# Performance work log

Measured on AMD Instinct MI355X. Metric: run time of the kernel, lower is better.

## Reference

```python
import jax, jax.numpy as jnp
import numpy as np

SCORE_THRESH = 0.05
NMS_THRESH = 0.5
MAX_DET = 100
N_BOXES = 8192


def setup_inputs() -> dict:
    key = jax.random.key(0)
    k1, k2, k3, k4, k5 = jax.random.split(key, 5)
    N = N_BOXES
    # well-formed axis-aligned boxes (x1,y1,x2,y2) plus 8 keypoint coords
    xy = jax.random.uniform(k1, (N, 2)) * 1000.0
    wh = jax.random.uniform(k2, (N, 2)) * 120.0 + 4.0
    kp = jax.random.uniform(k3, (N, 8)) * 1000.0
    boxes = jnp.concatenate([xy, xy + wh, kp], axis=1)            # (N, 12)
    classification = jax.random.uniform(k4, (N, 8))               # two heads x 4 orientations
    dimensions = jax.random.uniform(k5, (N, 3)) * 4.0             # (h, w, l) for the single class
    return {"boxes": boxes, "dimensions": dimensions, "classification": classification}


def _nms_keep(b4, scores, valid):
    """Greedy NMS. Returns (order, keep) where order sorts by score desc and
    keep[i] says whether the i-th sorted box survives."""
    N = b4.shape[0]
    order = jnp.argsort(-jnp.where(valid, scores, -jnp.inf))
    bs = b4[order]                                                 # (N, 4) sorted boxes
    vs = valid[order]
    x1, y1, x2, y2 = bs[:, 0], bs[:, 1], bs[:, 2], bs[:, 3]
    area = (x2 - x1) * (y2 - y1)
    iw = jnp.clip(jnp.minimum(x2[:, None], x2[None, :]) - jnp.maximum(x1[:, None], x1[None, :]), 0.0)
    ih = jnp.clip(jnp.minimum(y2[:, None], y2[None, :]) - jnp.maximum(y1[:, None], y1[None, :]), 0.0)
    inter = iw * ih                                                # (N, N)
    iou = inter / jnp.maximum(area[:, None] + area[None, :] - inter, 1e-8)
    idx = jnp.arange(N)

    def body(keep, xs):
        row, v, i = xs
        suppressed = jnp.any(keep & (row > NMS_THRESH) & (idx < i))
        keep = keep.at[i].set(v & jnp.logical_not(suppressed))
        return keep, None

    keep, _ = jax.lax.scan(body, jnp.zeros((N,), dtype=bool), (iou, vs, idx))
    return order, keep


def reference(boxes, dimensions, classification):
    # max over the two classification heads -> per-orientation score (N, 4)
    cls2 = jnp.maximum(classification[:, :4], classification[:, 4:])
    orient = jnp.argmax(cls2, axis=1)                              # best orientation per box
    score = jnp.max(cls2, axis=1)                                  # best-orientation score
    valid = score > SCORE_THRESH

    order, keep = _nms_keep(boxes[:, :4], score, valid)
    sorted_score = jnp.where(keep, score[order], -jnp.inf)
    top_scores, top_pos = jax.lax.top_k(sorted_score, MAX_DET)     # top-k among kept
    sel = order[top_pos]                                           # original box indices
    ok = jnp.isfinite(top_scores)                                  # real detections vs -1 padding

    out_boxes = jnp.where(ok[:, None], boxes[sel], -1.0)           # (MAX_DET, 12)
    out_dims = jnp.where(ok[:, None], dimensions[sel, :3], -1.0)   # (MAX_DET, 3)
    out_scores = jnp.where(ok, score[sel], -1.0)                   # (MAX_DET,)
    out_labels = jnp.where(ok, 0, -1).astype(jnp.int32)            # single class -> label 0
    out_orient = jnp.where(ok, orient[sel], -1).astype(jnp.int32)
    return out_boxes, out_dims, out_scores, out_labels, out_orient
```

## Files before the change

### kernel.cpp

```cpp
#include <hip/hip_runtime.h>

#define NBOX 8192
#define BT 1024
#define MAXDET 100
#define SCORE_T 0.05f
#define NMS_T 0.5f
#define CAP 1024
#define KTGT 128
#define TOPBIN_T 0.99609375f

typedef unsigned long long u64;

__device__ __forceinline__ float rl_f(float v, int j) {
    return __int_as_float(__builtin_amdgcn_readlane(__float_as_int(v), j));
}

__device__ __forceinline__ float iou_fn(float x1, float y1, float x2, float y2, float area,
                                        float bx1, float by1, float bx2, float by2, float barea) {
    float iw = fminf(x2, bx2) - fmaxf(x1, bx1);
    float ih = fminf(y2, by2) - fmaxf(y1, by1);
    iw = fmaxf(iw, 0.0f);
    ih = fmaxf(ih, 0.0f);
    float inter = iw * ih;
    return inter / fmaxf(area + barea - inter, 1e-8f);
}

__device__ __forceinline__ void bins_of(unsigned k, int& b1, int& b2) {
    float s = __uint_as_float(k & 0x7FFFFFFFu);
    b1 = (int)(s * 256.0f); if (b1 > 255) b1 = 255;
    b2 = (int)(s * 65536.0f) & 255;
}

__global__ __launch_bounds__(BT) void filterdet_kernel(
    const float* __restrict__ boxes, const float* __restrict__ dims,
    const float* __restrict__ cls, float* __restrict__ out) {
    __shared__ unsigned s_key[NBOX];
    __shared__ unsigned s_hist[256];
    __shared__ u64 s_sel[CAP];
    __shared__ u64 s_srt[CAP];
    __shared__ unsigned short s_srtpos[CAP];
    __shared__ float4 s_cb[CAP];
    __shared__ float4 s_bb[128];
    __shared__ float s_bar[128];
    __shared__ float4 s_kb[MAXDET];
    __shared__ float s_karea[MAXDET], s_kscore[MAXDET];
    __shared__ int s_ksel[MAXDET];
    __shared__ int s_kc, s_cnt, s_B1, s_B2, s_state, s_refKrem;
    __shared__ u64 s_alive0;

    const int tid = threadIdx.x;
    const int lane = tid & 63;
    const int wid = tid >> 6;

    auto rank_scatter = [&](int sc, bool loadBox) {
        if (tid < sc) {
            u64 mine = s_sel[tid];
            float4 pb = make_float4(0.f, 0.f, 0.f, 0.f);
            if (loadBox) {
                int bidx = NBOX - 1 - (int)(mine & 8191ull);
                pb = *reinterpret_cast<const float4*>(boxes + bidx * 12);
            }
            int rank = 0;
            int j = 0;
            for (; j + 8 <= sc; j += 8) {
                u64 a0 = s_sel[j + 0], a1 = s_sel[j + 1], a2 = s_sel[j + 2], a3 = s_sel[j + 3];
                u64 a4 = s_sel[j + 4], a5 = s_sel[j + 5], a6 = s_sel[j + 6], a7 = s_sel[j + 7];
                rank += (int)(a0 > mine) + (int)(a1 > mine) + (int)(a2 > mine) + (int)(a3 > mine)
                      + (int)(a4 > mine) + (int)(a5 > mine) + (int)(a6 > mine) + (int)(a7 > mine);
            }
            for (; j < sc; ++j) rank += (s_sel[j] > mine) ? 1 : 0;
            s_srt[rank] = mine;
            s_srtpos[rank] = (unsigned short)tid;
            if (loadBox) s_cb[tid] = pb;
        }
    };

    auto nms_groups = [&](int scN) {
        for (int base = 0; base < scN && s_kc < MAXDET; base += 128) {
            const int kc0 = s_kc;
            float x1 = 0.f, y1 = 0.f, x2 = 0.f, y2 = 0.f, area = 0.f, sscore = 0.f;
            int sidx = 0; bool have = false;
            if (wid < 2) {
                int p = base + wid * 64 + lane;
                have = p < scN;
                u64 v = have ? s_srt[p] : 0ull;
                int cp = have ? (int)s_srtpos[p] : 0;
                sidx = NBOX - 1 - (int)(v & 8191ull);
                sscore = __uint_as_float(((unsigned)(v >> 13)) & 0x7FFFFFFFu);
                float4 b = s_cb[cp];
                if (have) { x1 = b.x; y1 = b.y; x2 = b.z; y2 = b.w; area = (x2 - x1) * (y2 - y1); }
                int sl = wid * 64 + lane;
                s_bb[sl] = make_float4(x1, y1, x2, y2); s_bar[sl] = area;
            }
            __syncthreads();
            if (wid == 0) {
                bool cand = have;
                for (int k = 0; k < kc0; ++k) {
                    float4 kb = s_kb[k];
                    float iou = iou_fn(x1, y1, x2, y2, area, kb.x, kb.y, kb.z, kb.w, s_karea[k]);
                    cand = cand && !(iou > NMS_T);
                }
                u64 m = 0ull;
#pragma unroll 8
                for (int j = 0; j < 64; ++j) {
                    float iou = iou_fn(x1, y1, x2, y2, area,
                                       rl_f(x1, j), rl_f(y1, j), rl_f(x2, j), rl_f(y2, j), rl_f(area, j));
                    if ((iou > NMS_T) && (j < lane)) m |= (1ull << j);
                }
                u64 alive = __ballot(cand);
                u64 conf = __ballot((m & alive) != 0ull) & alive;
                while (conf) {
                    int i = (int)__builtin_ctzll(conf);
                    bool deadI = (lane == i) && ((m & alive) != 0ull);
                    u64 d = __ballot(deadI);
                    alive &= ~d; conf &= ~(d | (1ull << i));
                }
                int rank = (int)__popcll(alive & ((1ull << lane) - 1ull));
                int slot = kc0 + rank;
                if (((alive >> lane) & 1ull) && slot < MAXDET) {
                    s_kb[slot] = make_float4(x1, y1, x2, y2);
                    s_karea[slot] = area; s_kscore[slot] = sscore; s_ksel[slot] = sidx;
                }
                if (lane == 0) s_alive0 = alive;
            }
            u64 m_low = 0ull, m_high = 0ull;
            bool cand1 = have;
            if (wid == 1) {
                for (int k = 0; k < kc0; ++k) {
                    float4 kb = s_kb[k];
                    float iou = iou_fn(x1, y1, x2, y2, area, kb.x, kb.y, kb.z, kb.w, s_karea[k]);
                    cand1 = cand1 && !(iou > NMS_T);
                }
#pragma unroll 8
                for (int j = 0; j < 64; ++j) {
                    float4 bb = s_bb[j];
                    float iou = iou_fn(x1, y1, x2, y2, area, bb.x, bb.y, bb.z, bb.w, s_bar[j]);
                    if (iou > NMS_T) m_low |= (1ull << j);
                }
#pragma unroll 8
                for (int j = 0; j < 64; ++j) {
                    float iou = iou_fn(x1, y1, x2, y2, area,
                                       rl_f(x1, j), rl_f(y1, j), rl_f(x2, j), rl_f(y2, j), rl_f(area, j));
                    if ((iou > NMS_T) && (j < lane)) m_high |= (1ull << j);
                }
            }
            __syncthreads();
            if (wid == 1) {
                u64 alive0 = s_alive0;
                int popc0 = (int)__popcll(alive0);
                bool cand = cand1 && ((m_low & alive0) == 0ull);
                u64 alive = __ballot(cand);
                u64 conf = __ballot((m_high & alive) != 0ull) & alive;
                while (conf) {
                    int i = (int)__builtin_ctzll(conf);
                    bool deadI = (lane == i) && ((m_high & alive) != 0ull);
                    u64 d = __ballot(deadI);
                    alive &= ~d; conf &= ~(d | (1ull << i));
                }
                int rank = (int)__popcll(alive & ((1ull << lane) - 1ull));
                int slot = kc0 + popc0 + rank;
                if (((alive >> lane) & 1ull) && slot < MAXDET) {
                    s_kb[slot] = make_float4(x1, y1, x2, y2);
                    s_karea[slot] = area; s_kscore[slot] = sscore; s_ksel[slot] = sidx;
                }
                if (lane == 0) {
                    int nk = kc0 + popc0 + (int)__popcll(alive);
                    s_kc = nk > MAXDET ? MAXDET : nk;
                }
            }
            __syncthreads();
        }
    };

    unsigned keyr[8];
#pragma unroll
    for (int j = 0; j < 8; ++j) {
        int i = tid + j * BT;
        const float4 c0 = *reinterpret_cast<const float4*>(cls + i * 8);
        const float4 c1 = *reinterpret_cast<const float4*>(cls + i * 8 + 4);
        float s = fmaxf(fmaxf(fmaxf(c0.x, c1.x), fmaxf(c0.y, c1.y)),
                        fmaxf(fmaxf(c0.z, c1.z), fmaxf(c0.w, c1.w)));
        unsigned u = __float_as_uint(s);
        unsigned key = (u >> 31) ? ~u : (u | 0x80000000u);
        key = (s > SCORE_T) ? key : 0u;
        keyr[j] = key;
        s_key[i] = key;
    }
    if (tid == 0) { s_kc = 0; s_cnt = 0; }
    __syncthreads();
#pragma unroll
    for (int j = 0; j < 8; ++j) {
        unsigned k = keyr[j];
        if (k) {
            float s = __uint_as_float(k & 0x7FFFFFFFu);
            if (s >= TOPBIN_T) {
                int pos = atomicAdd(&s_cnt, 1);
                if (pos < CAP) {
                    int i = tid + j * BT;
                    s_sel[pos] = (((u64)k) << 13) | (unsigned)(NBOX - 1 - i);
                    s_cb[pos] = *reinterpret_cast<const float4*>(boxes + i * 12);
                }
            }
        }
    }
    __syncthreads();
    const int cnt0 = s_cnt;
    const bool ovf = cnt0 > CAP;

    if (!ovf && cnt0 > 0) {
        rank_scatter(cnt0, false);
        __syncthreads();
        nms_groups(cnt0);
    }

    int U1 = ovf ? 256 : 255;
    int U2 = 0;

    if (s_kc < MAXDET) {
        if (tid < 256) s_hist[tid] = 0u;
        if (tid == 0) s_cnt = 0;
        __syncthreads();
        for (int j = 0; j < NBOX / BT; ++j) {
            unsigned k = s_key[tid + j * BT];
            if (k) {
                int b1, b2; bins_of(k, b1, b2);
                if (b1 < U1 || (b1 == U1 && b2 < U2)) atomicAdd(&s_hist[b1], 1u);
            }
        }
        while (true) {
            __syncthreads();
            if (wid == 0) {
                unsigned c0 = s_hist[lane * 4 + 0], c1s = s_hist[lane * 4 + 1];
                unsigned c2 = s_hist[lane * 4 + 2], c3 = s_hist[lane * 4 + 3];
                unsigned t3 = c3, t2 = c2 + t3, t1 = c1s + t2, t0 = c0 + t1;
                unsigned acc = t0;
#pragma unroll
                for (int d = 1; d < 64; d <<= 1) {
                    unsigned o = __shfl_down(acc, d);
                    if (lane + d < 64) acc += o;
                }
                unsigned excl = acc - t0;
                unsigned totalRem = __shfl(acc, 0);
                if (lane == 0) s_state = (totalRem == 0u) ? 2 : 0;
                if (totalRem != 0u) {
                    unsigned Kt = totalRem < (unsigned)KTGT ? totalRem : (unsigned)KTGT;
                    unsigned incq[4] = { excl + t0, excl + t1, excl + t2, excl + t3 };
                    unsigned abvq[4] = { excl + t1, excl + t2, excl + t3, excl };
#pragma unroll
                    for (int q = 0; q < 4; ++q) {
                        if (incq[q] >= Kt && abvq[q] < Kt) {
                            s_B1 = lane * 4 + q; s_B2 = 0;
                            if (incq[q] > CAP) { s_state = 1; s_refKrem = (int)(Kt - abvq[q]); }
                        }
                    }
                }
            }
            __syncthreads();
            const int st = s_state;
            if (st == 2) break;
            const int B1 = s_B1;
            if (st == 1) {
                if (tid < 256) s_hist[tid] = 0u;
                __syncthreads();
                for (int j = 0; j < NBOX / BT; ++j) {
                    unsigned k = s_key[tid + j * BT];
                    if (k) {
                        int b1, b2; bins_of(k, b1, b2);
                        if ((b1 < U1 || (b1 == U1 && b2 < U2)) && b1 == B1)
                            atomicAdd(&s_hist[b2], 1u);
                    }
                }
                __syncthreads();
                if (wid == 0) {
                    unsigned c0 = s_hist[lane * 4 + 0], c1s = s_hist[lane * 4 + 1];
                    unsigned c2 = s_hist[lane * 4 + 2], c3 = s_hist[lane * 4 + 3];
                    unsigned t3 = c3, t2 = c2 + t3, t1 = c1s + t2, t0 = c0 + t1;
                    unsigned acc = t0;
#pragma unroll
                    for (int d = 1; d < 64; d <<= 1) {
                        unsigned o = __shfl_down(acc, d);
                        if (lane + d < 64) acc += o;
                    }
                    unsigned excl = acc - t0;
                    unsigned Krem = (unsigned)s_refKrem;
                    unsigned incq[4] = { excl + t0, excl + t1, excl + t2, excl + t3 };
                    unsigned abvq[4] = { excl + t1, excl + t2, excl + t3, excl };
#pragma unroll
                    for (int q = 0; q < 4; ++q)
                        if (incq[q] >= Krem && abvq[q] < Krem) s_B2 = lane * 4 + q;
                }
                __syncthreads();
            }
            const int B2 = s_B2;
            for (int j = 0; j < NBOX / BT; ++j) {
                int i = tid + j * BT;
                unsigned k = s_key[i];
                if (k) {
                    int b1, b2; bins_of(k, b1, b2);
                    bool inr = (b1 < U1) || (b1 == U1 && b2 < U2);
                    bool sel = inr && ((b1 > B1) || (b1 == B1 && b2 >= B2));
                    if (sel) {
                        int pos = atomicAdd(&s_cnt, 1);
                        if (pos < CAP)
                            s_sel[pos] = (((u64)k) << 13) | (unsigned)(NBOX - 1 - i);
                    }
                }
            }
            __syncthreads();
            const int sc2 = s_cnt < CAP ? s_cnt : CAP;
            rank_scatter(sc2, true);
            __syncthreads();
            nms_groups(sc2);
            if (s_kc >= MAXDET) break;
            U1 = B1; U2 = B2;
            if (tid < 256) s_hist[tid] = 0u;
            if (tid == 0) s_cnt = 0;
            __syncthreads();
            for (int j = 0; j < NBOX / BT; ++j) {
                unsigned k = s_key[tid + j * BT];
                if (k) {
                    int b1, b2; bins_of(k, b1, b2);
                    if (b1 < U1 || (b1 == U1 && b2 < U2)) atomicAdd(&s_hist[b1], 1u);
                }
            }
        }
    }
    __syncthreads();

    if (tid < MAXDET) {
        const int kc = s_kc;
        float* ob = out;
        float* od = out + MAXDET * 12;
        float* os = out + MAXDET * 15;
        float* ol = out + MAXDET * 16;
        float* oo = out + MAXDET * 17;
        float4* obr = reinterpret_cast<float4*>(ob + tid * 12);
        if (tid < kc) {
            int sel = s_ksel[tid];
            const float4* br = reinterpret_cast<const float4*>(boxes + sel * 12);
            obr[0] = br[0]; obr[1] = br[1]; obr[2] = br[2];
            od[tid * 3 + 0] = dims[sel * 3 + 0];
            od[tid * 3 + 1] = dims[sel * 3 + 1];
            od[tid * 3 + 2] = dims[sel * 3 + 2];
            os[tid] = s_kscore[tid];
            ol[tid] = 0.0f;
            const float4 c0 = *reinterpret_cast<const float4*>(cls + sel * 8);
            const float4 c1 = *reinterpret_cast<const float4*>(cls + sel * 8 + 4);
            float m0 = fmaxf(c0.x, c1.x);
            float m1 = fmaxf(c0.y, c1.y);
            float m2 = fmaxf(c0.z, c1.z);
            float m3 = fmaxf(c0.w, c1.w);
            int o = 0; float best = m0;
            if (m1 > best) { best = m1; o = 1; }
            if (m2 > best) { best = m2; o = 2; }
            if (m3 > best) { best = m3; o = 3; }
            oo[tid] = (float)o;
        } else {
            const float4 neg1 = make_float4(-1.f, -1.f, -1.f, -1.f);
            obr[0] = neg1; obr[1] = neg1; obr[2] = neg1;
            od[tid * 3 + 0] = -1.0f; od[tid * 3 + 1] = -1.0f; od[tid * 3 + 2] = -1.0f;
            os[tid] = -1.0f; ol[tid] = -1.0f; oo[tid] = -1.0f;
        }
    }
}

extern "C" void kernel_launch(void* const* d_in, const int* in_sizes, int n_in,
                              void* d_out, int out_size, void* d_ws, size_t ws_size,
                              hipStream_t stream) {
    const float* boxes = (const float*)d_in[0];
    const float* dims  = (const float*)d_in[1];
    const float* cls   = (const float*)d_in[2];
    float* out = (float*)d_out;
    (void)in_sizes; (void)n_in; (void)out_size; (void)d_ws; (void)ws_size;
    filterdet_kernel<<<1, BT, 0, stream>>>(boxes, dims, cls, out);
}
```

Baseline: 27.01 us.

## Split scoring into a multi-block prepass kernel and shrink the NMS kernel

Moves the per-box score/key computation and top-bin candidate compaction into a 64-block prepass kernel that writes keys, per-block counts, packed candidate keys, boxes, keypoints and dims/orientation to workspace. The single-block NMS kernel drops to 256 threads, prefix-sums the block counts to gather candidates, and emits outputs from the staged workspace arrays. The aim is to spread the global-memory-bound scoring pass across many CUs instead of one workgroup. The cost is an extra kernel launch and a global round trip, and the fallback histogram passes now run with a quarter of the threads.

```diff
diff --git a/kernel.cpp b/kernel.cpp
--- a/kernel.cpp
+++ b/kernel.cpp
@@ -1,15 +1,23 @@
 #include <hip/hip_runtime.h>
 
 #define NBOX 8192
-#define BT 1024
 #define MAXDET 100
 #define SCORE_T 0.05f
 #define NMS_T 0.5f
 #define CAP 1024
 #define KTGT 128
 #define TOPBIN_T 0.99609375f
+#define BT2 256
 
 typedef unsigned long long u64;
+
+#define WS_KEYS 0u
+#define WS_CNTS 32768u
+#define WS_KIDX 36864u
+#define WS_B0   102400u
+#define WS_KP0  233472u
+#define WS_KP1  364544u
+#define WS_DD   495616u
 
 __device__ __forceinline__ float rl_f(float v, int j) {
     return __int_as_float(__builtin_amdgcn_readlane(__float_as_int(v), j));
@@ -31,11 +39,54 @@
     b2 = (int)(s * 65536.0f) & 255;
 }
 
-__global__ __launch_bounds__(BT) void filterdet_kernel(
+__global__ __launch_bounds__(128) void score_push_kernel(
     const float* __restrict__ boxes, const float* __restrict__ dims,
-    const float* __restrict__ cls, float* __restrict__ out) {
+    const float* __restrict__ cls, unsigned* __restrict__ keys,
+    unsigned* __restrict__ cnts, u64* __restrict__ kidx,
+    float4* __restrict__ b0a, float4* __restrict__ kp0a,
+    float4* __restrict__ kp1a, float4* __restrict__ dda) {
+    __shared__ int s_lcnt;
+    const int t = threadIdx.x, blk = blockIdx.x;
+    const int i = blk * 128 + t;
+    if (t == 0) s_lcnt = 0;
+    __syncthreads();
+    const float4 c0 = *reinterpret_cast<const float4*>(cls + i * 8);
+    const float4 c1 = *reinterpret_cast<const float4*>(cls + i * 8 + 4);
+    float m0 = fmaxf(c0.x, c1.x), m1 = fmaxf(c0.y, c1.y);
+    float m2 = fmaxf(c0.z, c1.z), m3 = fmaxf(c0.w, c1.w);
+    float s = fmaxf(fmaxf(m0, m1), fmaxf(m2, m3));
+    unsigned u = __float_as_uint(s);
+    unsigned key = (u >> 31) ? ~u : (u | 0x80000000u);
+    key = (s > SCORE_T) ? key : 0u;
+    keys[i] = key;
+    if (key && s >= TOPBIN_T) {
+        int o = 0; float best = m0;
+        if (m1 > best) { best = m1; o = 1; }
+        if (m2 > best) { best = m2; o = 2; }
+        if (m3 > best) { best = m3; o = 3; }
+        int pos = atomicAdd(&s_lcnt, 1);
+        int slot = blk * 128 + pos;
+        kidx[slot] = (((u64)key) << 27) | (((u64)(NBOX - 1 - i)) << 14) | (unsigned)slot;
+        const float4* br = reinterpret_cast<const float4*>(boxes + i * 12);
+        b0a[slot] = br[0];
+        kp0a[slot] = br[1];
+        kp1a[slot] = br[2];
+        dda[slot] = make_float4(dims[i * 3], dims[i * 3 + 1], dims[i * 3 + 2], (float)o);
+    }
+    __syncthreads();
+    if (t == 0) cnts[blk] = (unsigned)s_lcnt;
+}
+
+__global__ __launch_bounds__(BT2) void nms_out_kernel(
+    const float* __restrict__ boxes, const float* __restrict__ dims,
+    const float* __restrict__ cls, const unsigned* __restrict__ keysG,
+    const unsigned* __restrict__ cnts, const u64* __restrict__ kidxG,
+    const float4* __restrict__ b0a, const float4* __restrict__ kp0a,
+    const float4* __restrict__ kp1a, const float4* __restrict__ dda,
+    float* __restrict__ out) {
     __shared__ unsigned s_key[NBOX];
     __shared__ unsigned s_hist[256];
+    __shared__ unsigned s_off[65];
     __shared__ u64 s_sel[CAP];
     __shared__ u64 s_srt[CAP];
     __shared__ unsigned short s_srtpos[CAP];
@@ -43,8 +94,8 @@
     __shared__ float4 s_bb[128];
     __shared__ float s_bar[128];
     __shared__ float4 s_kb[MAXDET];
-    __shared__ float s_karea[MAXDET], s_kscore[MAXDET];
-    __shared__ int s_ksel[MAXDET];
+    __shared__ float s_karea[MAXDET];
+    __shared__ u64 s_kv[MAXDET];
     __shared__ int s_kc, s_cnt, s_B1, s_B2, s_state, s_refKrem;
     __shared__ u64 s_alive0;
 
@@ -53,11 +104,11 @@
     const int wid = tid >> 6;
 
     auto rank_scatter = [&](int sc, bool loadBox) {
-        if (tid < sc) {
-            u64 mine = s_sel[tid];
+        for (int t = tid; t < sc; t += BT2) {
+            u64 mine = s_sel[t];
             float4 pb = make_float4(0.f, 0.f, 0.f, 0.f);
             if (loadBox) {
-                int bidx = NBOX - 1 - (int)(mine & 8191ull);
+                int bidx = NBOX - 1 - (int)((mine >> 14) & 8191ull);
                 pb = *reinterpret_cast<const float4*>(boxes + bidx * 12);
             }
             int rank = 0;
@@ -70,23 +121,21 @@
             }
             for (; j < sc; ++j) rank += (s_sel[j] > mine) ? 1 : 0;
             s_srt[rank] = mine;
-            s_srtpos[rank] = (unsigned short)tid;
-            if (loadBox) s_cb[tid] = pb;
+            s_srtpos[rank] = (unsigned short)t;
+            if (loadBox) s_cb[t] = pb;
         }
     };
 
     auto nms_groups = [&](int scN) {
         for (int base = 0; base < scN && s_kc < MAXDET; base += 128) {
             const int kc0 = s_kc;
-            float x1 = 0.f, y1 = 0.f, x2 = 0.f, y2 = 0.f, area = 0.f, sscore = 0.f;
-            int sidx = 0; bool have = false;
+            float x1 = 0.f, y1 = 0.f, x2 = 0.f, y2 = 0.f, area = 0.f;
+            u64 v = 0ull; bool have = false;
             if (wid < 2) {
                 int p = base + wid * 64 + lane;
                 have = p < scN;
-                u64 v = have ? s_srt[p] : 0ull;
+                v = have ? s_srt[p] : 0ull;
                 int cp = have ? (int)s_srtpos[p] : 0;
-                sidx = NBOX - 1 - (int)(v & 8191ull);
-                sscore = __uint_as_float(((unsigned)(v >> 13)) & 0x7FFFFFFFu);
                 float4 b = s_cb[cp];
                 if (have) { x1 = b.x; y1 = b.y; x2 = b.z; y2 = b.w; area = (x2 - x1) * (y2 - y1); }
                 int sl = wid * 64 + lane;
@@ -119,7 +168,7 @@
                 int slot = kc0 + rank;
                 if (((alive >> lane) & 1ull) && slot < MAXDET) {
                     s_kb[slot] = make_float4(x1, y1, x2, y2);
-                    s_karea[slot] = area; s_kscore[slot] = sscore; s_ksel[slot] = sidx;
+                    s_karea[slot] = area; s_kv[slot] = v;
                 }
                 if (lane == 0) s_alive0 = alive;
             }
@@ -161,7 +210,7 @@
                 int slot = kc0 + popc0 + rank;
                 if (((alive >> lane) & 1ull) && slot < MAXDET) {
                     s_kb[slot] = make_float4(x1, y1, x2, y2);
-                    s_karea[slot] = area; s_kscore[slot] = sscore; s_ksel[slot] = sidx;
+                    s_karea[slot] = area; s_kv[slot] = v;
                 }
                 if (lane == 0) {
                     int nk = kc0 + popc0 + (int)__popcll(alive);
@@ -172,56 +221,53 @@
         }
     };
 
-    unsigned keyr[8];
-#pragma unroll
-    for (int j = 0; j < 8; ++j) {
-        int i = tid + j * BT;
-        const float4 c0 = *reinterpret_cast<const float4*>(cls + i * 8);
-        const float4 c1 = *reinterpret_cast<const float4*>(cls + i * 8 + 4);
-        float s = fmaxf(fmaxf(fmaxf(c0.x, c1.x), fmaxf(c0.y, c1.y)),
-                        fmaxf(fmaxf(c0.z, c1.z), fmaxf(c0.w, c1.w)));
-        unsigned u = __float_as_uint(s);
-        unsigned key = (u >> 31) ? ~u : (u | 0x80000000u);
-        key = (s > SCORE_T) ? key : 0u;
-        keyr[j] = key;
-        s_key[i] = key;
-    }
     if (tid == 0) { s_kc = 0; s_cnt = 0; }
-    __syncthreads();
-#pragma unroll
-    for (int j = 0; j < 8; ++j) {
-        unsigned k = keyr[j];
-        if (k) {
-            float s = __uint_as_float(k & 0x7FFFFFFFu);
-            if (s >= TOPBIN_T) {
-                int pos = atomicAdd(&s_cnt, 1);
-                if (pos < CAP) {
-                    int i = tid + j * BT;
-                    s_sel[pos] = (((u64)k) << 13) | (unsigned)(NBOX - 1 - i);
-                    s_cb[pos] = *reinterpret_cast<const float4*>(boxes + i * 12);
-                }
-            }
-        }
+    if (wid == 0) {
+        unsigned acc = cnts[lane];
+#pragma unroll
+        for (int d = 1; d < 64; d <<= 1) {
+            unsigned o = __shfl_up(acc, d);
+            if (lane >= d) acc += o;
+        }
+        s_off[lane + 1] = acc;
+        if (lane == 0) s_off[0] = 0u;
     }
     __syncthreads();
-    const int cnt0 = s_cnt;
-    const bool ovf = cnt0 > CAP;
-
-    if (!ovf && cnt0 > 0) {
-        rank_scatter(cnt0, false);
+    const int sc = (int)s_off[64];
+    const bool fast = (sc > 0 && sc <= CAP);
+
+    if (fast) {
+        const int r = tid >> 2;
+        const unsigned o_r = s_off[r];
+        const int c_r = (int)(s_off[r + 1] - o_r);
+        for (int j = (tid & 3); j < c_r; j += 4) {
+            int g = r * 128 + j;
+            int dst = (int)o_r + j;
+            s_sel[dst] = kidxG[g];
+            s_cb[dst] = b0a[g];
+        }
         __syncthreads();
-        nms_groups(cnt0);
+        rank_scatter(sc, false);
+        __syncthreads();
+        nms_groups(sc);
     }
-
-    int U1 = ovf ? 256 : 255;
+    __syncthreads();
+
+    int U1 = fast ? 255 : (sc == 0 ? 255 : 256);
     int U2 = 0;
 
     if (s_kc < MAXDET) {
-        if (tid < 256) s_hist[tid] = 0u;
+        {
+            const uint4* kp = reinterpret_cast<const uint4*>(keysG);
+            uint4* sk = reinterpret_cast<uint4*>(s_key);
+#pragma unroll
+            for (int j = 0; j < NBOX / 4 / BT2; ++j) sk[tid + j * BT2] = kp[tid + j * BT2];
+        }
+        s_hist[tid] = 0u;
         if (tid == 0) s_cnt = 0;
         __syncthreads();
-        for (int j = 0; j < NBOX / BT; ++j) {
-            unsigned k = s_key[tid + j * BT];
+        for (int j = 0; j < NBOX / BT2; ++j) {
+            unsigned k = s_key[tid + j * BT2];
             if (k) {
                 int b1, b2; bins_of(k, b1, b2);
                 if (b1 < U1 || (b1 == U1 && b2 < U2)) atomicAdd(&s_hist[b1], 1u);
@@ -260,10 +306,10 @@
             if (st == 2) break;
             const int B1 = s_B1;
             if (st == 1) {
-                if (tid < 256) s_hist[tid] = 0u;
+                s_hist[tid] = 0u;
                 __syncthreads();
-                for (int j = 0; j < NBOX / BT; ++j) {
-                    unsigned k = s_key[tid + j * BT];
+                for (int j = 0; j < NBOX / BT2; ++j) {
+                    unsigned k = s_key[tid + j * BT2];
                     if (k) {
                         int b1, b2; bins_of(k, b1, b2);
                         if ((b1 < U1 || (b1 == U1 && b2 < U2)) && b1 == B1)
@@ -292,8 +338,8 @@
                 __syncthreads();
             }
             const int B2 = s_B2;
-            for (int j = 0; j < NBOX / BT; ++j) {
-                int i = tid + j * BT;
+            for (int j = 0; j < NBOX / BT2; ++j) {
+                int i = tid + j * BT2;
                 unsigned k = s_key[i];
                 if (k) {
                     int b1, b2; bins_of(k, b1, b2);
@@ -302,7 +348,7 @@
                     if (sel) {
                         int pos = atomicAdd(&s_cnt, 1);
                         if (pos < CAP)
-                            s_sel[pos] = (((u64)k) << 13) | (unsigned)(NBOX - 1 - i);
+                            s_sel[pos] = (((u64)k) << 27) | (((u64)(NBOX - 1 - i)) << 14) | 0x3FFFull;
                     }
                 }
             }
@@ -313,11 +359,11 @@
             nms_groups(sc2);
             if (s_kc >= MAXDET) break;
             U1 = B1; U2 = B2;
-            if (tid < 256) s_hist[tid] = 0u;
+            s_hist[tid] = 0u;
             if (tid == 0) s_cnt = 0;
             __syncthreads();
-            for (int j = 0; j < NBOX / BT; ++j) {
-                unsigned k = s_key[tid + j * BT];
+            for (int j = 0; j < NBOX / BT2; ++j) {
+                unsigned k = s_key[tid + j * BT2];
                 if (k) {
                     int b1, b2; bins_of(k, b1, b2);
                     if (b1 < U1 || (b1 == U1 && b2 < U2)) atomicAdd(&s_hist[b1], 1u);
@@ -336,25 +382,35 @@
         float* oo = out + MAXDET * 17;
         float4* obr = reinterpret_cast<float4*>(ob + tid * 12);
         if (tid < kc) {
-            int sel = s_ksel[tid];
-            const float4* br = reinterpret_cast<const float4*>(boxes + sel * 12);
-            obr[0] = br[0]; obr[1] = br[1]; obr[2] = br[2];
-            od[tid * 3 + 0] = dims[sel * 3 + 0];
-            od[tid * 3 + 1] = dims[sel * 3 + 1];
-            od[tid * 3 + 2] = dims[sel * 3 + 2];
-            os[tid] = s_kscore[tid];
+            u64 v = s_kv[tid];
+            float sscore = __uint_as_float(((unsigned)(v >> 27)) & 0x7FFFFFFFu);
+            unsigned low = (unsigned)(v & 16383ull);
+            obr[0] = s_kb[tid];
+            os[tid] = sscore;
             ol[tid] = 0.0f;
-            const float4 c0 = *reinterpret_cast<const float4*>(cls + sel * 8);
-            const float4 c1 = *reinterpret_cast<const float4*>(cls + sel * 8 + 4);
-            float m0 = fmaxf(c0.x, c1.x);
-            float m1 = fmaxf(c0.y, c1.y);
-            float m2 = fmaxf(c0.z, c1.z);
-            float m3 = fmaxf(c0.w, c1.w);
-            int o = 0; float best = m0;
-            if (m1 > best) { best = m1; o = 1; }
-            if (m2 > best) { best = m2; o = 2; }
-            if (m3 > best) { best = m3; o = 3; }
-            oo[tid] = (float)o;
+            if (low < 8192u) {
+                obr[1] = kp0a[low];
+                obr[2] = kp1a[low];
+                float4 dd = dda[low];
+                od[tid * 3 + 0] = dd.x; od[tid * 3 + 1] = dd.y; od[tid * 3 + 2] = dd.z;
+                oo[tid] = dd.w;
+            } else {
+                int idx = NBOX - 1 - (int)((v >> 14) & 8191ull);
+                const float4* br = reinterpret_cast<const float4*>(boxes + idx * 12);
+                obr[1] = br[1]; obr[2] = br[2];
+                od[tid * 3 + 0] = dims[idx * 3 + 0];
+                od[tid * 3 + 1] = dims[idx * 3 + 1];
+                od[tid * 3 + 2] = dims[idx * 3 + 2];
+                const float4 c0 = *reinterpret_cast<const float4*>(cls + idx * 8);
+                const float4 c1 = *reinterpret_cast<const float4*>(cls + idx * 8 + 4);
+                float m0 = fmaxf(c0.x, c1.x), m1 = fmaxf(c0.y, c1.y);
+                float m2 = fmaxf(c0.z, c1.z), m3 = fmaxf(c0.w, c1.w);
+                int o = 0; float best = m0;
+                if (m1 > best) { best = m1; o = 1; }
+                if (m2 > best) { best = m2; o = 2; }
+                if (m3 > best) { best = m3; o = 3; }
+                oo[tid] = (float)o;
+            }
         } else {
             const float4 neg1 = make_float4(-1.f, -1.f, -1.f, -1.f);
             obr[0] = neg1; obr[1] = neg1; obr[2] = neg1;
@@ -371,6 +427,15 @@
     const float* dims  = (const float*)d_in[1];
     const float* cls   = (const float*)d_in[2];
     float* out = (float*)d_out;
-    (void)in_sizes; (void)n_in; (void)out_size; (void)d_ws; (void)ws_size;
-    filterdet_kernel<<<1, BT, 0, stream>>>(boxes, dims, cls, out);
-}
+    unsigned char* ws = (unsigned char*)d_ws;
+    unsigned* keys = (unsigned*)(ws + WS_KEYS);
+    unsigned* cnts = (unsigned*)(ws + WS_CNTS);
+    u64* kidx      = (u64*)(ws + WS_KIDX);
+    float4* b0a    = (float4*)(ws + WS_B0);
+    float4* kp0a   = (float4*)(ws + WS_KP0);
+    float4* kp1a   = (float4*)(ws + WS_KP1);
+    float4* dda    = (float4*)(ws + WS_DD);
+    (void)in_sizes; (void)n_in; (void)out_size; (void)ws_size;
+    score_push_kernel<<<NBOX / 128, 128, 0, stream>>>(boxes, dims, cls, keys, cnts, kidx, b0a, kp0a, kp1a, dda);
+    nms_out_kernel<<<1, BT2, 0, stream>>>(boxes, dims, cls, keys, cnts, kidx, b0a, kp0a, kp1a, dda, out);
+}
```

After: 27.94 us. +3.5%, slower.

## Add fast-path kernel with parallel bitmask NMS over top-bin candidates and fallback

Applied to the files above, without the earlier changes.

Adds a fast-path kernel that gathers only boxes whose score falls in the top bin, builds pairwise suppression and score-order bitmasks, and resolves greedy NMS by iterating parallel keep/dead decisions until none are undecided. It writes outputs directly by rank when at least MAXDET boxes survive. Otherwise it sets a workspace flag, and the original histogram-based kernel runs as a second launch guarded by that flag. This aims to replace the serial grouped NMS in the common case, at the cost of a second kernel launch and a workspace flag round-trip.

```diff
diff --git a/kernel.cpp b/kernel.cpp
--- a/kernel.cpp
+++ b/kernel.cpp
@@ -6,6 +6,8 @@
 #define SCORE_T 0.05f
 #define NMS_T 0.5f
 #define CAP 1024
+#define CAPM 384
+#define NWMAX 6
 #define KTGT 128
 #define TOPBIN_T 0.99609375f
 
@@ -31,9 +33,158 @@
     b2 = (int)(s * 65536.0f) & 255;
 }
 
-__global__ __launch_bounds__(BT) void filterdet_kernel(
+__global__ __launch_bounds__(BT) void hot_kernel(
     const float* __restrict__ boxes, const float* __restrict__ dims,
-    const float* __restrict__ cls, float* __restrict__ out) {
+    const float* __restrict__ cls, unsigned* __restrict__ flagG,
+    float* __restrict__ out) {
+    __shared__ u64 s_sel[CAPM];
+    __shared__ float4 s_cb[CAPM];
+    __shared__ unsigned char s_or[CAPM];
+    __shared__ u64 s_gt[NWMAX][CAPM];
+    __shared__ u64 s_sg[NWMAX][CAPM];
+    __shared__ u64 s_K[NWMAX], s_U[NWMAX];
+    __shared__ int s_cnt;
+
+    const int tid = threadIdx.x;
+    const int lane = tid & 63;
+    const int w = tid >> 6;
+
+    if (tid == 0) s_cnt = 0;
+    __syncthreads();
+
+#pragma unroll
+    for (int j = 0; j < NBOX / BT; ++j) {
+        int i = tid + j * BT;
+        const float4 c0 = *reinterpret_cast<const float4*>(cls + i * 8);
+        const float4 c1 = *reinterpret_cast<const float4*>(cls + i * 8 + 4);
+        float m0 = fmaxf(c0.x, c1.x), m1 = fmaxf(c0.y, c1.y);
+        float m2 = fmaxf(c0.z, c1.z), m3 = fmaxf(c0.w, c1.w);
+        float s = fmaxf(fmaxf(m0, m1), fmaxf(m2, m3));
+        if (s > SCORE_T && s >= TOPBIN_T) {
+            unsigned u = __float_as_uint(s);
+            unsigned key = (u >> 31) ? ~u : (u | 0x80000000u);
+            int o = 0; float best = m0;
+            if (m1 > best) { best = m1; o = 1; }
+            if (m2 > best) { best = m2; o = 2; }
+            if (m3 > best) { best = m3; o = 3; }
+            int pos = atomicAdd(&s_cnt, 1);
+            if (pos < CAPM) {
+                s_sel[pos] = (((u64)key) << 13) | (unsigned)(NBOX - 1 - i);
+                s_cb[pos] = *reinterpret_cast<const float4*>(boxes + i * 12);
+                s_or[pos] = (unsigned char)o;
+            }
+        }
+    }
+    __syncthreads();
+    const int cnt = s_cnt;
+    if (cnt == 0 || cnt > CAPM) {
+        if (tid == 0) flagG[0] = 1u;
+        return;
+    }
+    const int NW = (cnt + 63) >> 6;
+
+    const int tot = NW * cnt;
+    for (int p = tid; p < tot; p += BT) {
+        int q = p / cnt;
+        int t = p - q * cnt;
+        u64 selt = s_sel[t];
+        float4 bt = s_cb[t];
+        float x1 = bt.x, y1 = bt.y, x2 = bt.z, y2 = bt.w;
+        float area = (x2 - x1) * (y2 - y1);
+        int jbase = q << 6;
+        int jmax = cnt - jbase; if (jmax > 64) jmax = 64;
+        u64 g = 0ull, sg = 0ull;
+        for (int jj = 0; jj < jmax; ++jj) {
+            int jdx = jbase + jj;
+            u64 selj = s_sel[jdx];
+            float4 bj = s_cb[jdx];
+            float barea = (bj.z - bj.x) * (bj.w - bj.y);
+            float iou = iou_fn(x1, y1, x2, y2, area, bj.x, bj.y, bj.z, bj.w, barea);
+            if (selj > selt) {
+                u64 bit = 1ull << jj;
+                g |= bit;
+                if (iou > NMS_T) sg |= bit;
+            }
+        }
+        s_gt[q][t] = g;
+        s_sg[q][t] = sg;
+    }
+    if (tid < NWMAX) {
+        int base = tid << 6;
+        u64 uw = (cnt <= base) ? 0ull
+               : ((cnt - base >= 64) ? ~0ull : ((1ull << (cnt - base)) - 1ull));
+        s_U[tid] = uw;
+        s_K[tid] = 0ull;
+    }
+    __syncthreads();
+
+    const int t = tid;
+    const bool have = t < cnt;
+    for (int it = 0; it < CAPM; ++it) {
+        bool undec = have && ((s_U[t >> 6] >> (t & 63)) & 1ull);
+        u64 deadm = 0ull, blkm = 0ull;
+        if (undec) {
+            for (int q = 0; q < NW; ++q) {
+                u64 sg = s_sg[q][t];
+                deadm |= sg & s_K[q];
+                blkm  |= sg & s_U[q];
+            }
+        }
+        bool toDead = undec && (deadm != 0ull);
+        bool toKept = undec && (deadm == 0ull) && (blkm == 0ull);
+        u64 dW = __ballot(toDead);
+        u64 kW = __ballot(toKept);
+        if (lane == 0 && w < NW) {
+            s_K[w] |= kW;
+            s_U[w] &= ~(kW | dW);
+        }
+        __syncthreads();
+        u64 anyU = 0ull;
+        for (int q = 0; q < NW; ++q) anyU |= s_U[q];
+        if (anyU == 0ull) break;
+        __syncthreads();
+    }
+
+    int kcnt = 0;
+    for (int q = 0; q < NW; ++q) kcnt += (int)__popcll(s_K[q]);
+    if (kcnt < MAXDET) {
+        if (tid == 0) flagG[0] = 1u;
+        return;
+    }
+    if (tid == 0) flagG[0] = 0u;
+
+    float* ob = out;
+    float* od = out + MAXDET * 12;
+    float* os = out + MAXDET * 15;
+    float* ol = out + MAXDET * 16;
+    float* oo = out + MAXDET * 17;
+    if (have && ((s_K[t >> 6] >> (t & 63)) & 1ull)) {
+        int rank = 0;
+        for (int q = 0; q < NW; ++q) rank += (int)__popcll(s_gt[q][t] & s_K[q]);
+        if (rank < MAXDET) {
+            u64 v = s_sel[t];
+            int idx = NBOX - 1 - (int)(v & 8191ull);
+            float sscore = __uint_as_float(((unsigned)(v >> 13)) & 0x7FFFFFFFu);
+            float4* obr = reinterpret_cast<float4*>(ob + rank * 12);
+            const float4* br = reinterpret_cast<const float4*>(boxes + idx * 12);
+            obr[0] = s_cb[t];
+            obr[1] = br[1];
+            obr[2] = br[2];
+            od[rank * 3 + 0] = dims[idx * 3 + 0];
+            od[rank * 3 + 1] = dims[idx * 3 + 1];
+            od[rank * 3 + 2] = dims[idx * 3 + 2];
+            os[rank] = sscore;
+            ol[rank] = 0.0f;
+            oo[rank] = (float)s_or[t];
+        }
+    }
+}
+
+__global__ __launch_bounds__(BT) void fallback_kernel(
+    const float* __restrict__ boxes, const float* __restrict__ dims,
+    const float* __restrict__ cls, const unsigned* __restrict__ flagG,
+    float* __restrict__ out) {
+    if (flagG[0] == 0u) return;
     __shared__ unsigned s_key[NBOX];
     __shared__ unsigned s_hist[256];
     __shared__ u64 s_sel[CAP];
@@ -174,7 +325,7 @@
 
     unsigned keyr[8];
 #pragma unroll
-    for (int j = 0; j < 8; ++j) {
+    for (int j = 0; j < NBOX / BT; ++j) {
         int i = tid + j * BT;
         const float4 c0 = *reinterpret_cast<const float4*>(cls + i * 8);
         const float4 c1 = *reinterpret_cast<const float4*>(cls + i * 8 + 4);
@@ -189,7 +340,7 @@
     if (tid == 0) { s_kc = 0; s_cnt = 0; }
     __syncthreads();
 #pragma unroll
-    for (int j = 0; j < 8; ++j) {
+    for (int j = 0; j < NBOX / BT; ++j) {
         unsigned k = keyr[j];
         if (k) {
             float s = __uint_as_float(k & 0x7FFFFFFFu);
@@ -206,16 +357,13 @@
     __syncthreads();
     const int cnt0 = s_cnt;
     const bool ovf = cnt0 > CAP;
-
     if (!ovf && cnt0 > 0) {
         rank_scatter(cnt0, false);
         __syncthreads();
         nms_groups(cnt0);
     }
-
     int U1 = ovf ? 256 : 255;
     int U2 = 0;
-
     if (s_kc < MAXDET) {
         if (tid < 256) s_hist[tid] = 0u;
         if (tid == 0) s_cnt = 0;
@@ -326,7 +474,6 @@
         }
     }
     __syncthreads();
-
     if (tid < MAXDET) {
         const int kc = s_kc;
         float* ob = out;
@@ -346,10 +493,8 @@
             ol[tid] = 0.0f;
             const float4 c0 = *reinterpret_cast<const float4*>(cls + sel * 8);
             const float4 c1 = *reinterpret_cast<const float4*>(cls + sel * 8 + 4);
-            float m0 = fmaxf(c0.x, c1.x);
-            float m1 = fmaxf(c0.y, c1.y);
-            float m2 = fmaxf(c0.z, c1.z);
-            float m3 = fmaxf(c0.w, c1.w);
+            float m0 = fmaxf(c0.x, c1.x), m1 = fmaxf(c0.y, c1.y);
+            float m2 = fmaxf(c0.z, c1.z), m3 = fmaxf(c0.w, c1.w);
             int o = 0; float best = m0;
             if (m1 > best) { best = m1; o = 1; }
             if (m2 > best) { best = m2; o = 2; }
@@ -371,6 +516,8 @@
     const float* dims  = (const float*)d_in[1];
     const float* cls   = (const float*)d_in[2];
     float* out = (float*)d_out;
-    (void)in_sizes; (void)n_in; (void)out_size; (void)d_ws; (void)ws_size;
-    filterdet_kernel<<<1, BT, 0, stream>>>(boxes, dims, cls, out);
+    unsigned* flag = (unsigned*)d_ws;
+    (void)in_sizes; (void)n_in; (void)out_size; (void)ws_size;
+    hot_kernel<<<1, BT, 0, stream>>>(boxes, dims, cls, flag, out);
+    fallback_kernel<<<1, BT, 0, stream>>>(boxes, dims, cls, flag, out);
 }
```

Measured after the change: 27.74 us. +2.7%, slower.

## Prefetch top-bin payload into LDS, wave-aggregate atomics, split rank counting

Applied to the files above, without the earlier changes.

During the initial scoring pass, candidates in the top score bin are compacted with one atomic per wavefront. Their full box, keypoints, dimensions and orientation are staged into shared memory, so the final output write avoids dependent global gathers. The first-pass rank computation is split across 4 threads per candidate with atomic accumulation, which shortens the serial comparison loop. The cost is a smaller capacity (384) for the fast path, more shared memory, extra global loads for candidates that may never be output, and per-slot bookkeeping to fall back to global reads.

```diff
diff --git a/kernel.cpp b/kernel.cpp
--- a/kernel.cpp
+++ b/kernel.cpp
@@ -6,6 +6,7 @@
 #define SCORE_T 0.05f
 #define NMS_T 0.5f
 #define CAP 1024
+#define CAPM 384
 #define KTGT 128
 #define TOPBIN_T 0.99609375f
 
@@ -40,11 +41,15 @@
     __shared__ u64 s_srt[CAP];
     __shared__ unsigned short s_srtpos[CAP];
     __shared__ float4 s_cb[CAP];
+    __shared__ float4 s_pay[CAPM][3];
+    __shared__ unsigned char s_orr[CAPM];
+    __shared__ int s_rank[CAPM];
     __shared__ float4 s_bb[128];
     __shared__ float s_bar[128];
     __shared__ float4 s_kb[MAXDET];
-    __shared__ float s_karea[MAXDET], s_kscore[MAXDET];
-    __shared__ int s_ksel[MAXDET];
+    __shared__ float s_karea[MAXDET];
+    __shared__ u64 s_kv[MAXDET];
+    __shared__ unsigned short s_kcp[MAXDET];
     __shared__ int s_kc, s_cnt, s_B1, s_B2, s_state, s_refKrem;
     __shared__ u64 s_alive0;
 
@@ -52,41 +57,16 @@
     const int lane = tid & 63;
     const int wid = tid >> 6;
 
-    auto rank_scatter = [&](int sc, bool loadBox) {
-        if (tid < sc) {
-            u64 mine = s_sel[tid];
-            float4 pb = make_float4(0.f, 0.f, 0.f, 0.f);
-            if (loadBox) {
-                int bidx = NBOX - 1 - (int)(mine & 8191ull);
-                pb = *reinterpret_cast<const float4*>(boxes + bidx * 12);
-            }
-            int rank = 0;
-            int j = 0;
-            for (; j + 8 <= sc; j += 8) {
-                u64 a0 = s_sel[j + 0], a1 = s_sel[j + 1], a2 = s_sel[j + 2], a3 = s_sel[j + 3];
-                u64 a4 = s_sel[j + 4], a5 = s_sel[j + 5], a6 = s_sel[j + 6], a7 = s_sel[j + 7];
-                rank += (int)(a0 > mine) + (int)(a1 > mine) + (int)(a2 > mine) + (int)(a3 > mine)
-                      + (int)(a4 > mine) + (int)(a5 > mine) + (int)(a6 > mine) + (int)(a7 > mine);
-            }
-            for (; j < sc; ++j) rank += (s_sel[j] > mine) ? 1 : 0;
-            s_srt[rank] = mine;
-            s_srtpos[rank] = (unsigned short)tid;
-            if (loadBox) s_cb[tid] = pb;
-        }
-    };
-
-    auto nms_groups = [&](int scN) {
+    auto nms_groups = [&](int scN, bool hasPay) {
         for (int base = 0; base < scN && s_kc < MAXDET; base += 128) {
             const int kc0 = s_kc;
-            float x1 = 0.f, y1 = 0.f, x2 = 0.f, y2 = 0.f, area = 0.f, sscore = 0.f;
-            int sidx = 0; bool have = false;
+            float x1 = 0.f, y1 = 0.f, x2 = 0.f, y2 = 0.f, area = 0.f;
+            u64 v = 0ull; int cp = 0; bool have = false;
             if (wid < 2) {
                 int p = base + wid * 64 + lane;
                 have = p < scN;
-                u64 v = have ? s_srt[p] : 0ull;
-                int cp = have ? (int)s_srtpos[p] : 0;
-                sidx = NBOX - 1 - (int)(v & 8191ull);
-                sscore = __uint_as_float(((unsigned)(v >> 13)) & 0x7FFFFFFFu);
+                v = have ? s_srt[p] : 0ull;
+                cp = have ? (int)s_srtpos[p] : 0;
                 float4 b = s_cb[cp];
                 if (have) { x1 = b.x; y1 = b.y; x2 = b.z; y2 = b.w; area = (x2 - x1) * (y2 - y1); }
                 int sl = wid * 64 + lane;
@@ -119,7 +99,8 @@
                 int slot = kc0 + rank;
                 if (((alive >> lane) & 1ull) && slot < MAXDET) {
                     s_kb[slot] = make_float4(x1, y1, x2, y2);
-                    s_karea[slot] = area; s_kscore[slot] = sscore; s_ksel[slot] = sidx;
+                    s_karea[slot] = area; s_kv[slot] = v;
+                    s_kcp[slot] = hasPay ? (unsigned short)cp : (unsigned short)0xFFFF;
                 }
                 if (lane == 0) s_alive0 = alive;
             }
@@ -161,7 +142,8 @@
                 int slot = kc0 + popc0 + rank;
                 if (((alive >> lane) & 1ull) && slot < MAXDET) {
                     s_kb[slot] = make_float4(x1, y1, x2, y2);
-                    s_karea[slot] = area; s_kscore[slot] = sscore; s_ksel[slot] = sidx;
+                    s_karea[slot] = area; s_kv[slot] = v;
+                    s_kcp[slot] = hasPay ? (unsigned short)cp : (unsigned short)0xFFFF;
                 }
                 if (lane == 0) {
                     int nk = kc0 + popc0 + (int)__popcll(alive);
@@ -172,51 +154,98 @@
         }
     };
 
-    unsigned keyr[8];
+    if (tid == 0) { s_kc = 0; s_cnt = 0; }
+    if (tid < CAPM) s_rank[tid] = 0;
+    __syncthreads();
+
 #pragma unroll
-    for (int j = 0; j < 8; ++j) {
+    for (int j = 0; j < NBOX / BT; ++j) {
         int i = tid + j * BT;
         const float4 c0 = *reinterpret_cast<const float4*>(cls + i * 8);
         const float4 c1 = *reinterpret_cast<const float4*>(cls + i * 8 + 4);
-        float s = fmaxf(fmaxf(fmaxf(c0.x, c1.x), fmaxf(c0.y, c1.y)),
-                        fmaxf(fmaxf(c0.z, c1.z), fmaxf(c0.w, c1.w)));
+        float m0 = fmaxf(c0.x, c1.x), m1 = fmaxf(c0.y, c1.y);
+        float m2 = fmaxf(c0.z, c1.z), m3 = fmaxf(c0.w, c1.w);
+        float s = fmaxf(fmaxf(m0, m1), fmaxf(m2, m3));
         unsigned u = __float_as_uint(s);
         unsigned key = (u >> 31) ? ~u : (u | 0x80000000u);
         key = (s > SCORE_T) ? key : 0u;
-        keyr[j] = key;
         s_key[i] = key;
-    }
-    if (tid == 0) { s_kc = 0; s_cnt = 0; }
-    __syncthreads();
-#pragma unroll
-    for (int j = 0; j < 8; ++j) {
-        unsigned k = keyr[j];
-        if (k) {
-            float s = __uint_as_float(k & 0x7FFFFFFFu);
-            if (s >= TOPBIN_T) {
-                int pos = atomicAdd(&s_cnt, 1);
-                if (pos < CAP) {
-                    int i = tid + j * BT;
-                    s_sel[pos] = (((u64)k) << 13) | (unsigned)(NBOX - 1 - i);
-                    s_cb[pos] = *reinterpret_cast<const float4*>(boxes + i * 12);
-                }
+        bool isc = (key != 0u) && (s >= TOPBIN_T);
+        u64 bal = __ballot(isc);
+        int nb = (int)__popcll(bal);
+        int b = 0;
+        if (lane == 0 && nb) b = atomicAdd(&s_cnt, nb);
+        b = __shfl(b, 0);
+        if (isc) {
+            int pos = b + (int)__popcll(bal & ((1ull << lane) - 1ull));
+            if (pos < CAPM) {
+                int o = 0; float best = m0;
+                if (m1 > best) { best = m1; o = 1; }
+                if (m2 > best) { best = m2; o = 2; }
+                if (m3 > best) { best = m3; o = 3; }
+                s_sel[pos] = (((u64)key) << 13) | (unsigned)(NBOX - 1 - i);
+                s_orr[pos] = (unsigned char)o;
+                const float4* br = reinterpret_cast<const float4*>(boxes + i * 12);
+                s_cb[pos] = br[0];
+                s_pay[pos][0] = br[1];
+                s_pay[pos][1] = br[2];
+                s_pay[pos][2] = make_float4(dims[i * 3], dims[i * 3 + 1], dims[i * 3 + 2], 0.f);
             }
         }
     }
     __syncthreads();
     const int cnt0 = s_cnt;
-    const bool ovf = cnt0 > CAP;
+    const bool ovf = cnt0 > CAPM;
 
     if (!ovf && cnt0 > 0) {
-        rank_scatter(cnt0, false);
+        const int sc = cnt0;
+        const int p = tid & 3;
+        const int chunk = (sc + 3) >> 2;
+        const int j0 = p * chunk;
+        int j1 = j0 + chunk; if (j1 > sc) j1 = sc;
+        for (int c = tid >> 2; c < sc; c += 256) {
+            u64 mine = s_sel[c];
+            int r = 0;
+            int j = j0;
+            for (; j + 8 <= j1; j += 8) {
+                u64 a0 = s_sel[j + 0], a1 = s_sel[j + 1], a2 = s_sel[j + 2], a3 = s_sel[j + 3];
+                u64 a4 = s_sel[j + 4], a5 = s_sel[j + 5], a6 = s_sel[j + 6], a7 = s_sel[j + 7];
+                r += (int)(a0 > mine) + (int)(a1 > mine) + (int)(a2 > mine) + (int)(a3 > mine)
+                   + (int)(a4 > mine) + (int)(a5 > mine) + (int)(a6 > mine) + (int)(a7 > mine);
+            }
+            for (; j < j1; ++j) r += (s_sel[j] > mine) ? 1 : 0;
+            if (r) atomicAdd(&s_rank[c], r);
+        }
         __syncthreads();
-        nms_groups(cnt0);
+        if (tid < sc) { int rk = s_rank[tid]; s_srt[rk] = s_sel[tid]; s_srtpos[rk] = (unsigned short)tid; }
+        __syncthreads();
+        nms_groups(sc, true);
     }
 
     int U1 = ovf ? 256 : 255;
     int U2 = 0;
 
     if (s_kc < MAXDET) {
+        auto rank_scatter = [&](int sc) {
+            if (tid < sc) {
+                u64 mine = s_sel[tid];
+                int bidx = NBOX - 1 - (int)(mine & 8191ull);
+                float4 pb = *reinterpret_cast<const float4*>(boxes + bidx * 12);
+                int rank = 0;
+                int j = 0;
+                for (; j + 8 <= sc; j += 8) {
+                    u64 a0 = s_sel[j + 0], a1 = s_sel[j + 1], a2 = s_sel[j + 2], a3 = s_sel[j + 3];
+                    u64 a4 = s_sel[j + 4], a5 = s_sel[j + 5], a6 = s_sel[j + 6], a7 = s_sel[j + 7];
+                    rank += (int)(a0 > mine) + (int)(a1 > mine) + (int)(a2 > mine) + (int)(a3 > mine)
+                          + (int)(a4 > mine) + (int)(a5 > mine) + (int)(a6 > mine) + (int)(a7 > mine);
+                }
+                for (; j < sc; ++j) rank += (s_sel[j] > mine) ? 1 : 0;
+                s_srt[rank] = mine;
+                s_srtpos[rank] = (unsigned short)tid;
+                s_cb[tid] = pb;
+            }
+        };
+
         if (tid < 256) s_hist[tid] = 0u;
         if (tid == 0) s_cnt = 0;
         __syncthreads();
@@ -308,9 +337,9 @@
             }
             __syncthreads();
             const int sc2 = s_cnt < CAP ? s_cnt : CAP;
-            rank_scatter(sc2, true);
-            __syncthreads();
-            nms_groups(sc2);
+            rank_scatter(sc2);
+            __syncthreads();
+            nms_groups(sc2, false);
             if (s_kc >= MAXDET) break;
             U1 = B1; U2 = B2;
             if (tid < 256) s_hist[tid] = 0u;
@@ -324,6 +353,7 @@
                 }
             }
         }
+        __syncthreads();
     }
     __syncthreads();
 
@@ -336,25 +366,35 @@
         float* oo = out + MAXDET * 17;
         float4* obr = reinterpret_cast<float4*>(ob + tid * 12);
         if (tid < kc) {
-            int sel = s_ksel[tid];
-            const float4* br = reinterpret_cast<const float4*>(boxes + sel * 12);
-            obr[0] = br[0]; obr[1] = br[1]; obr[2] = br[2];
-            od[tid * 3 + 0] = dims[sel * 3 + 0];
-            od[tid * 3 + 1] = dims[sel * 3 + 1];
-            od[tid * 3 + 2] = dims[sel * 3 + 2];
-            os[tid] = s_kscore[tid];
+            u64 v = s_kv[tid];
+            float sscore = __uint_as_float(((unsigned)(v >> 13)) & 0x7FFFFFFFu);
+            int cp = (int)s_kcp[tid];
+            obr[0] = s_kb[tid];
+            os[tid] = sscore;
             ol[tid] = 0.0f;
-            const float4 c0 = *reinterpret_cast<const float4*>(cls + sel * 8);
-            const float4 c1 = *reinterpret_cast<const float4*>(cls + sel * 8 + 4);
-            float m0 = fmaxf(c0.x, c1.x);
-            float m1 = fmaxf(c0.y, c1.y);
-            float m2 = fmaxf(c0.z, c1.z);
-            float m3 = fmaxf(c0.w, c1.w);
-            int o = 0; float best = m0;
-            if (m1 > best) { best = m1; o = 1; }
-            if (m2 > best) { best = m2; o = 2; }
-            if (m3 > best) { best = m3; o = 3; }
-            oo[tid] = (float)o;
+            if (cp != 0xFFFF) {
+                obr[1] = s_pay[cp][0];
+                obr[2] = s_pay[cp][1];
+                float4 dd = s_pay[cp][2];
+                od[tid * 3 + 0] = dd.x; od[tid * 3 + 1] = dd.y; od[tid * 3 + 2] = dd.z;
+                oo[tid] = (float)s_orr[cp];
+            } else {
+                int idx = NBOX - 1 - (int)(v & 8191ull);
+                const float4* br = reinterpret_cast<const float4*>(boxes + idx * 12);
+                obr[1] = br[1]; obr[2] = br[2];
+                od[tid * 3 + 0] = dims[idx * 3 + 0];
+                od[tid * 3 + 1] = dims[idx * 3 + 1];
+                od[tid * 3 + 2] = dims[idx * 3 + 2];
+                const float4 c0 = *reinterpret_cast<const float4*>(cls + idx * 8);
+                const float4 c1 = *reinterpret_cast<const float4*>(cls + idx * 8 + 4);
+                float m0 = fmaxf(c0.x, c1.x), m1 = fmaxf(c0.y, c1.y);
+                float m2 = fmaxf(c0.z, c1.z), m3 = fmaxf(c0.w, c1.w);
+                int o = 0; float best = m0;
+                if (m1 > best) { best = m1; o = 1; }
+                if (m2 > best) { best = m2; o = 2; }
+                if (m3 > best) { best = m3; o = 3; }
+                oo[tid] = (float)o;
+            }
         } else {
             const float4 neg1 = make_float4(-1.f, -1.f, -1.f, -1.f);
             obr[0] = neg1; obr[1] = neg1; obr[2] = neg1;
```

Measured after the change: 26.47 us. 1.02x faster.
